# Kernel optimization log

Measured on AMD Instinct MI355X. Metric: run time of the kernel, lower is better.

## Reference

```python
import jax, jax.numpy as jnp
import numpy as np

CH_IN, CH_OUT, KH, KW = 64, 128, 3, 3


def setup_inputs() -> dict:
    key = jax.random.key(0)
    k1, k2, k3 = jax.random.split(key, 3)
    x = jax.random.normal(k1, (16, CH_IN, 256, 256), dtype=jnp.float32)
    W_hat = jax.random.normal(k2, (CH_OUT, CH_IN * KH * KW), dtype=jnp.float32)
    M_hat = jax.random.normal(k3, (CH_OUT, CH_IN * KH * KW), dtype=jnp.float32)
    return {"x": x, "W_hat": W_hat, "M_hat": M_hat}


def reference(x, W_hat, M_hat):
    # NAC weight transform, then a standard same-padded conv (no bias).
    # Patch flattening order in the original (narrow(-1)/narrow(-2) then reshape)
    # matches (C_in, KH, KW) conv weight layout.
    W = jnp.tanh(W_hat) * jax.nn.sigmoid(M_hat)          # [C_out, C_in*KH*KW]
    W = W.reshape(CH_OUT, CH_IN, KH, KW)                  # OIHW
    out = jax.lax.conv_general_dilated(
        x, W,
        window_strides=(1, 1),
        padding=((KH // 2, KH // 2), (KW // 2, KW // 2)),
        dimension_numbers=("NCHW", "OIHW", "NCHW"),
    )
    return out
```

## Files before the change

kernel.cpp:

```cpp
#include <hip/hip_runtime.h>
#include <hip/hip_bf16.h>
#include <stdint.h>


#define CH_IN  64
#define CH_OUT 128
#define HW     256
#define NBATCH 16

typedef __attribute__((ext_vector_type(8))) short short8;
typedef __attribute__((ext_vector_type(4))) float f32x4;

static __device__ __forceinline__ uint32_t pack_bf16(float a, float b) {
    uint32_t ua = __builtin_bit_cast(uint32_t, a);
    uint32_t ub = __builtin_bit_cast(uint32_t, b);
    ua = (ua + 0x7FFFu + ((ua >> 16) & 1u)) >> 16;
    ub = (ub + 0x7FFFu + ((ub >> 16) & 1u));
    return (ua & 0xFFFFu) | (ub & 0xFFFF0000u);
}

__global__ void __launch_bounds__(256) nac_prep(const float* __restrict__ Wh,
                                                const float* __restrict__ Mh,
                                                uint32_t* __restrict__ Af) {
    int f = blockIdx.x * 256 + threadIdx.x;
    if (f >= 9 * 8 * 2 * 64) return;
    int lane = f & 63;
    int s    = (f >> 6) & 1;
    int ms   = (f >> 7) & 7;
    int t    = f >> 10;
    int co   = ms * 16 + (lane & 15);
    int ci0  = s * 32 + ((lane >> 4) << 3);

    uint32_t pk[4];
#pragma unroll
    for (int j2 = 0; j2 < 4; ++j2) {
        int ci = ci0 + 2 * j2;
        int k0 = ci * 9 + t;
        int k1 = k0 + 9;
        float w0 = tanhf(Wh[co * 576 + k0]);
        float m0 = Mh[co * 576 + k0];
        float w1 = tanhf(Wh[co * 576 + k1]);
        float m1 = Mh[co * 576 + k1];
        float v0 = w0 * (1.0f / (1.0f + expf(-m0)));
        float v1 = w1 * (1.0f / (1.0f + expf(-m1)));
        pk[j2] = pack_bf16(v0, v1);
    }
    int fragidx = ((t * 8 + ms) * 2 + s) * 64 + lane;
    reinterpret_cast<uint4*>(Af)[fragidx] = make_uint4(pk[0], pk[1], pk[2], pk[3]);
}

__global__ void __launch_bounds__(256) nac_conv(const float* __restrict__ x,
                                                const uint32_t* __restrict__ Af,
                                                float* __restrict__ out) {
    __shared__ uint32_t xl[8 * 272 * 4];

    unsigned bid = blockIdx.x;
    unsigned idx = (bid & 7u) * 1024u + (bid >> 3);
    int ht = idx & 127;
    int wt = (idx >> 7) & 3;
    int n  = idx >> 9;
    int h0 = ht * 2;
    int w0 = wt * 64;

    int tid = threadIdx.x;

    const float* xn = x + (size_t)n * CH_IN * HW * HW;
    for (int it = 0; it < 9; ++it) {
        int task = tid + it * 256;
        if (task < 2176) {
            int r   = task / 544;
            int rem = task - r * 544;
            int pg  = rem / 68;
            int c   = rem - pg * 68;
            int hrow = h0 - 1 + r;
            int w    = w0 - 1 + c;
            float v[8];
            if ((unsigned)hrow < 256u && (unsigned)w < 256u) {
                const float* p = xn + ((size_t)(pg * 8) * HW + hrow) * HW + w;
#pragma unroll
                for (int e = 0; e < 8; ++e) v[e] = p[(size_t)e * HW * HW];
            } else {
#pragma unroll
                for (int e = 0; e < 8; ++e) v[e] = 0.0f;
            }
            uint4 wd;
            wd.x = pack_bf16(v[0], v[1]);
            wd.y = pack_bf16(v[2], v[3]);
            wd.z = pack_bf16(v[4], v[5]);
            wd.w = pack_bf16(v[6], v[7]);
            *reinterpret_cast<uint4*>(&xl[(pg * 272 + r * 68 + c) * 4]) = wd;
        }
    }
    __syncthreads();

    int lane = tid & 63;
    int wv   = tid >> 6;
    int wm   = wv >> 1;
    int wn   = wv & 1;
    int row4 = lane >> 4;
    int col  = lane & 15;

    f32x4 acc[4][4];
#pragma unroll
    for (int mi = 0; mi < 4; ++mi)
#pragma unroll
        for (int ni = 0; ni < 4; ++ni)
            acc[mi][ni] = (f32x4){0.f, 0.f, 0.f, 0.f};

    const short8* Afr = reinterpret_cast<const short8*>(Af);

    for (int t = 0; t < 9; ++t) {
        int kh = t / 3, kw = t % 3;
        short8 a[2][4];
#pragma unroll
        for (int s = 0; s < 2; ++s)
#pragma unroll
            for (int mi = 0; mi < 4; ++mi)
                a[s][mi] = Afr[((t * 8 + (wm * 4 + mi)) * 2 + s) * 64 + lane];

#pragma unroll
        for (int s = 0; s < 2; ++s) {
            short8 b[4];
#pragma unroll
            for (int ni = 0; ni < 4; ++ni) {
                int pg = s * 4 + row4;
                int pp = (wn + kh) * 68 + ni * 16 + col + kw;
                b[ni] = *reinterpret_cast<const short8*>(&xl[(pg * 272 + pp) * 4]);
            }
#pragma unroll
            for (int mi = 0; mi < 4; ++mi)
#pragma unroll
                for (int ni = 0; ni < 4; ++ni)
                    acc[mi][ni] = __builtin_amdgcn_mfma_f32_16x16x32_bf16(
                        a[s][mi], b[ni], acc[mi][ni], 0, 0, 0);
        }
    }

#pragma unroll
    for (int mi = 0; mi < 4; ++mi) {
#pragma unroll
        for (int reg = 0; reg < 4; ++reg) {
            int co = wm * 64 + mi * 16 + row4 * 4 + reg;
            float* op = out + (((size_t)n * CH_OUT + co) * HW + (h0 + wn)) * HW + w0;
#pragma unroll
            for (int ni = 0; ni < 4; ++ni)
                op[ni * 16 + col] = acc[mi][ni][reg];
        }
    }
}

extern "C" void kernel_launch(void* const* d_in, const int* in_sizes, int n_in,
                              void* d_out, int out_size, void* d_ws, size_t ws_size,
                              hipStream_t stream) {
    const float* x  = (const float*)d_in[0];
    const float* Wh = (const float*)d_in[1];
    const float* Mh = (const float*)d_in[2];
    float* out = (float*)d_out;
    uint32_t* Af = (uint32_t*)d_ws;

    nac_prep<<<36, 256, 0, stream>>>(Wh, Mh, Af);
    nac_conv<<<8192, 256, 0, stream>>>(x, Af, out);
}
```

Measured before the change: 333.0 us.

## Pre-convert input to channel-last bf16 and use 32x32 MFMA direct conv

Adds a separate pass that converts x from NCHW fp32 into an NHWC-packed bf16 buffer in workspace. A new conv kernel then reads B fragments straight from global memory, with weights staged in LDS through global_load_lds, and computes with 32x32x16 MFMA over a 4-row by 64-column tile split across two output-channel halves. This removes the per-block strided fp32 halo gather and repacking, but adds a full extra read and write of the input plus a workspace requirement. The old path is kept as a fallback when workspace is too small.

Measured after the change: 516.5 us. 1.55x slower.

```diff
diff --git a/kernel.cpp b/kernel.cpp
--- a/kernel.cpp
+++ b/kernel.cpp
@@ -6,10 +6,13 @@
 #define CH_IN  64
 #define CH_OUT 128
 #define HW     256
-#define NBATCH 16
-
-typedef __attribute__((ext_vector_type(8))) short short8;
-typedef __attribute__((ext_vector_type(4))) float f32x4;
+
+typedef __attribute__((ext_vector_type(8)))  short short8;
+typedef __attribute__((ext_vector_type(16))) float f32x16;
+typedef __attribute__((ext_vector_type(4)))  float f32x4;
+
+#define XB_BYTE  147456u
+#define WS_NEED  (147456ull + 134217728ull)
 
 static __device__ __forceinline__ uint32_t pack_bf16(float a, float b) {
     uint32_t ua = __builtin_bit_cast(uint32_t, a);
@@ -19,17 +22,17 @@
     return (ua & 0xFFFFu) | (ub & 0xFFFF0000u);
 }
 
-__global__ void __launch_bounds__(256) nac_prep(const float* __restrict__ Wh,
-                                                const float* __restrict__ Mh,
-                                                uint32_t* __restrict__ Af) {
+__global__ void __launch_bounds__(256) nac_prep32(const float* __restrict__ Wh,
+                                                  const float* __restrict__ Mh,
+                                                  uint32_t* __restrict__ Af) {
     int f = blockIdx.x * 256 + threadIdx.x;
-    if (f >= 9 * 8 * 2 * 64) return;
+    if (f >= 9 * 4 * 4 * 64) return;
     int lane = f & 63;
-    int s    = (f >> 6) & 1;
-    int ms   = (f >> 7) & 7;
+    int s    = (f >> 6) & 3;
+    int ms   = (f >> 8) & 3;
     int t    = f >> 10;
-    int co   = ms * 16 + (lane & 15);
-    int ci0  = s * 32 + ((lane >> 4) << 3);
+    int co   = ms * 32 + (lane & 31);
+    int ci0  = s * 16 + ((lane >> 5) << 3);
 
     uint32_t pk[4];
 #pragma unroll
@@ -45,15 +48,173 @@
         float v1 = w1 * (1.0f / (1.0f + expf(-m1)));
         pk[j2] = pack_bf16(v0, v1);
     }
+    int fragidx = ((t * 4 + ms) * 4 + s) * 64 + lane;
+    reinterpret_cast<uint4*>(Af)[fragidx] = make_uint4(pk[0], pk[1], pk[2], pk[3]);
+}
+
+__global__ void __launch_bounds__(256) nac_prep16(const float* __restrict__ Wh,
+                                                  const float* __restrict__ Mh,
+                                                  uint32_t* __restrict__ Af) {
+    int f = blockIdx.x * 256 + threadIdx.x;
+    if (f >= 9 * 8 * 2 * 64) return;
+    int lane = f & 63;
+    int s    = (f >> 6) & 1;
+    int ms   = (f >> 7) & 7;
+    int t    = f >> 10;
+    int co   = ms * 16 + (lane & 15);
+    int ci0  = s * 32 + ((lane >> 4) << 3);
+    uint32_t pk[4];
+#pragma unroll
+    for (int j2 = 0; j2 < 4; ++j2) {
+        int ci = ci0 + 2 * j2;
+        int k0 = ci * 9 + t;
+        int k1 = k0 + 9;
+        float w0 = tanhf(Wh[co * 576 + k0]);
+        float m0 = Mh[co * 576 + k0];
+        float w1 = tanhf(Wh[co * 576 + k1]);
+        float m1 = Mh[co * 576 + k1];
+        float v0 = w0 * (1.0f / (1.0f + expf(-m0)));
+        float v1 = w1 * (1.0f / (1.0f + expf(-m1)));
+        pk[j2] = pack_bf16(v0, v1);
+    }
     int fragidx = ((t * 8 + ms) * 2 + s) * 64 + lane;
     reinterpret_cast<uint4*>(Af)[fragidx] = make_uint4(pk[0], pk[1], pk[2], pk[3]);
 }
 
-__global__ void __launch_bounds__(256) nac_conv(const float* __restrict__ x,
-                                                const uint32_t* __restrict__ Af,
-                                                float* __restrict__ out) {
+__global__ void __launch_bounds__(256) nac_convert(const float* __restrict__ x,
+                                                   uint32_t* __restrict__ xb) {
+    int bid = blockIdx.x;
+    int h   = bid & 255;
+    int n   = bid >> 8;
+    int px  = threadIdx.x;
+    const float* xr = x + ((size_t)n * CH_IN * HW + h) * HW + px;
+    uint32_t* orow = xb + ((size_t)(n * HW + h) * HW + px) * 32;
+#pragma unroll
+    for (int g = 0; g < 8; ++g) {
+        float v0 = xr[(size_t)(g * 8 + 0) * HW * HW];
+        float v1 = xr[(size_t)(g * 8 + 1) * HW * HW];
+        float v2 = xr[(size_t)(g * 8 + 2) * HW * HW];
+        float v3 = xr[(size_t)(g * 8 + 3) * HW * HW];
+        float v4 = xr[(size_t)(g * 8 + 4) * HW * HW];
+        float v5 = xr[(size_t)(g * 8 + 5) * HW * HW];
+        float v6 = xr[(size_t)(g * 8 + 6) * HW * HW];
+        float v7 = xr[(size_t)(g * 8 + 7) * HW * HW];
+        uint4 wd;
+        wd.x = pack_bf16(v0, v1); wd.y = pack_bf16(v2, v3);
+        wd.z = pack_bf16(v4, v5); wd.w = pack_bf16(v6, v7);
+        *reinterpret_cast<uint4*>(orow + g * 4) = wd;
+    }
+}
+
+__global__ void __launch_bounds__(256, 4)
+nac_convd(const uint32_t* __restrict__ xb, const uint32_t* __restrict__ Af,
+          float* __restrict__ out) {
+    __shared__ __align__(1024) uint32_t al[36 * 256];
+
+    unsigned bid = blockIdx.x;
+    unsigned idx = (bid & 7u) * 1024u + (bid >> 3);
+    const int cosplit = idx & 1;
+    const int ht = (idx >> 1) & 63;
+    const int wt = (idx >> 7) & 3;
+    const int n  = idx >> 9;
+    const int h0 = ht * 4;
+    const int w0 = wt * 64;
+
+    const int tid   = threadIdx.x;
+    const int lane  = tid & 63;
+    const int wv    = tid >> 6;
+    const int col32 = lane & 31;
+    const int hi    = lane >> 5;
+    const int cib   = hi * 16;
+
+    const char* xbb = reinterpret_cast<const char*>(xb) + ((size_t)n << 23);
+    const char* lb  = reinterpret_cast<const char*>(al);
+
+    f32x16 acc[2][2];
+#pragma unroll
+    for (int mi = 0; mi < 2; ++mi)
+#pragma unroll
+        for (int ni = 0; ni < 2; ++ni)
+#pragma unroll
+            for (int r = 0; r < 16; ++r) acc[mi][ni][r] = 0.f;
+
+    const short8 zero8 = (short8){0, 0, 0, 0, 0, 0, 0, 0};
+
+#pragma unroll
+    for (int ph = 0; ph < 2; ++ph) {
+        if (ph) __syncthreads();
+
+#pragma unroll
+        for (int i = 0; i < 9; ++i) {
+            const int f  = wv * 9 + i;
+            const int t  = f >> 2;
+            const int mi = (f >> 1) & 1;
+            const int sl = f & 1;
+            const int gidx = ((t * 4 + (cosplit * 2 + mi)) * 4 + (ph * 2 + sl));
+            const uint32_t* src = Af + gidx * 256 + lane * 4;
+            __builtin_amdgcn_global_load_lds(
+                (const __attribute__((address_space(1))) uint32_t*)src,
+                (__attribute__((address_space(3))) uint32_t*)&al[f * 256],
+                16, 0, 0);
+        }
+        __syncthreads();
+
+        const int cio = ph * 64 + cib;
+
+#pragma unroll
+        for (int t = 0; t < 9; ++t) {
+            const int kh = t / 3, kw = t % 3;
+            const int hh = h0 + wv + kh - 1;
+            if ((unsigned)hh < 256u) {
+                const char* rp = xbb + ((size_t)hh << 15);
+#pragma unroll
+                for (int sl = 0; sl < 2; ++sl) {
+                    short8 a0 = *reinterpret_cast<const short8*>(
+                        lb + (t * 4 + 0 + sl) * 1024 + lane * 16);
+                    short8 a1 = *reinterpret_cast<const short8*>(
+                        lb + (t * 4 + 2 + sl) * 1024 + lane * 16);
+#pragma unroll
+                    for (int ni = 0; ni < 2; ++ni) {
+                        const int p = w0 + ni * 32 + col32 + kw - 1;
+                        short8 b;
+                        if ((kw == 0 && ni == 0) || (kw == 2 && ni == 1)) {
+                            const bool pv = (unsigned)p < 256u;
+                            const int  pc = pv ? p : (kw == 0 ? 0 : 255);
+                            b = *reinterpret_cast<const short8*>(
+                                rp + ((size_t)pc << 7) + cio + sl * 32);
+                            if (!pv) b = zero8;
+                        } else {
+                            b = *reinterpret_cast<const short8*>(
+                                rp + ((size_t)p << 7) + cio + sl * 32);
+                        }
+                        acc[0][ni] = __builtin_amdgcn_mfma_f32_32x32x16_bf16(
+                            a0, b, acc[0][ni], 0, 0, 0);
+                        acc[1][ni] = __builtin_amdgcn_mfma_f32_32x32x16_bf16(
+                            a1, b, acc[1][ni], 0, 0, 0);
+                    }
+                }
+            }
+        }
+    }
+
+    const int hrow = h0 + wv;
+    const size_t ob = ((size_t)n * CH_OUT) * 65536 + (size_t)hrow * 256 + w0;
+#pragma unroll
+    for (int mi = 0; mi < 2; ++mi)
+#pragma unroll
+        for (int r = 0; r < 16; ++r) {
+            const int co = cosplit * 64 + mi * 32 + (r & 3) + 8 * (r >> 2) + 4 * hi;
+            float* op = out + ob + (size_t)co * 65536;
+#pragma unroll
+            for (int ni = 0; ni < 2; ++ni)
+                op[ni * 32 + col32] = acc[mi][ni][r];
+        }
+}
+
+__global__ void __launch_bounds__(256) nac_conv_fb(const float* __restrict__ x,
+                                                   const uint32_t* __restrict__ Af,
+                                                   float* __restrict__ out) {
     __shared__ uint32_t xl[8 * 272 * 4];
-
     unsigned bid = blockIdx.x;
     unsigned idx = (bid & 7u) * 1024u + (bid >> 3);
     int ht = idx & 127;
@@ -61,7 +222,6 @@
     int n  = idx >> 9;
     int h0 = ht * 2;
     int w0 = wt * 64;
-
     int tid = threadIdx.x;
 
     const float* xn = x + (size_t)n * CH_IN * HW * HW;
@@ -104,11 +264,9 @@
 #pragma unroll
     for (int mi = 0; mi < 4; ++mi)
 #pragma unroll
-        for (int ni = 0; ni < 4; ++ni)
-            acc[mi][ni] = (f32x4){0.f, 0.f, 0.f, 0.f};
+        for (int ni = 0; ni < 4; ++ni) acc[mi][ni] = (f32x4){0.f, 0.f, 0.f, 0.f};
 
     const short8* Afr = reinterpret_cast<const short8*>(Af);
-
     for (int t = 0; t < 9; ++t) {
         int kh = t / 3, kw = t % 3;
         short8 a[2][4];
@@ -117,7 +275,6 @@
 #pragma unroll
             for (int mi = 0; mi < 4; ++mi)
                 a[s][mi] = Afr[((t * 8 + (wm * 4 + mi)) * 2 + s) * 64 + lane];
-
 #pragma unroll
         for (int s = 0; s < 2; ++s) {
             short8 b[4];
@@ -143,8 +300,7 @@
             int co = wm * 64 + mi * 16 + row4 * 4 + reg;
             float* op = out + (((size_t)n * CH_OUT + co) * HW + (h0 + wn)) * HW + w0;
 #pragma unroll
-            for (int ni = 0; ni < 4; ++ni)
-                op[ni * 16 + col] = acc[mi][ni][reg];
+            for (int ni = 0; ni < 4; ++ni) op[ni * 16 + col] = acc[mi][ni][reg];
         }
     }
 }
@@ -156,8 +312,16 @@
     const float* Wh = (const float*)d_in[1];
     const float* Mh = (const float*)d_in[2];
     float* out = (float*)d_out;
-    uint32_t* Af = (uint32_t*)d_ws;
-
-    nac_prep<<<36, 256, 0, stream>>>(Wh, Mh, Af);
-    nac_conv<<<8192, 256, 0, stream>>>(x, Af, out);
-}
+    uint32_t* ws32 = (uint32_t*)d_ws;
+    const uint32_t* Af = ws32;
+    uint32_t* xbuf = ws32 + XB_BYTE / 4;
+
+    if (ws_size >= WS_NEED) {
+        nac_prep32<<<36, 256, 0, stream>>>(Wh, Mh, ws32);
+        nac_convert<<<4096, 256, 0, stream>>>(x, xbuf);
+        nac_convd<<<8192, 256, 0, stream>>>(xbuf, Af, out);
+    } else {
+        nac_prep16<<<36, 256, 0, stream>>>(Wh, Mh, ws32);
+        nac_conv_fb<<<8192, 256, 0, stream>>>(x, Af, out);
+    }
+}
```
